# Kernel tuning notes

Measured on AMD Instinct MI355X. Metric: run time of the kernel, lower is better.

Reference implementation:

```python
import jax, jax.numpy as jnp
import numpy as np

HID = 768          # args.hidden_size
LSTM2 = 768        # args.lstm_dim * 2
SCALE = HID ** -0.5


def _cross_attn(q_in, kv_in, Wq, bq, Wk, bk, Wv, bv):
    # Linear projections (weights stored as [in, out])
    Q = q_in @ Wq + bq            # [B, Sq, H]
    K = kv_in @ Wk + bk           # [B, Sk, H]
    V = kv_in @ Wv + bv           # [B, Sk, H]
    attn = jnp.einsum('bqh,bkh->bqk', Q, K) * SCALE
    attn = jax.nn.softmax(attn, axis=-1)
    return jnp.einsum('bqk,bkh->bqh', attn, V)


def setup_inputs() -> dict:
    key = jax.random.key(0)
    ks = jax.random.split(key, 14)
    B, Ssyn, Ssem = 4, 4096, 2048
    syntactic_feat = jax.random.normal(ks[0], (B, Ssyn, LSTM2), jnp.float32)
    semantic_feat = jax.random.normal(ks[1], (B, Ssem, HID), jnp.float32)

    def lin(k, fan_in, fan_out):
        kw, kb = jax.random.split(k)
        bound = 1.0 / np.sqrt(fan_in)
        W = jax.random.uniform(kw, (fan_in, fan_out), jnp.float32, -bound, bound)
        b = jax.random.uniform(kb, (fan_out,), jnp.float32, -bound, bound)
        return W, b

    # syntax_to_semantic: query_dim=HID, key_dim=LSTM2
    Wq1, bq1 = lin(ks[2], HID, HID)
    Wk1, bk1 = lin(ks[3], LSTM2, HID)
    Wv1, bv1 = lin(ks[4], LSTM2, HID)
    # semantic_to_syntax: query_dim=LSTM2, key_dim=HID
    Wq2, bq2 = lin(ks[5], LSTM2, HID)
    Wk2, bk2 = lin(ks[6], HID, HID)
    Wv2, bv2 = lin(ks[7], HID, HID)
    return dict(syntactic_feat=syntactic_feat, semantic_feat=semantic_feat,
                Wq1=Wq1, bq1=bq1, Wk1=Wk1, bk1=bk1, Wv1=Wv1, bv1=bv1,
                Wq2=Wq2, bq2=bq2, Wk2=Wk2, bk2=bk2, Wv2=Wv2, bv2=bv2)


def reference(syntactic_feat, semantic_feat,
              Wq1, bq1, Wk1, bk1, Wv1, bv1,
              Wq2, bq2, Wk2, bk2, Wv2, bv2):
    # enhanced_semantic: queries from semantic, keys/values from syntactic
    enhanced_semantic = _cross_attn(semantic_feat, syntactic_feat,
                                    Wq1, bq1, Wk1, bk1, Wv1, bv1)
    # enhanced_syntax: queries from syntactic, keys/values from semantic
    enhanced_syntax = _cross_attn(syntactic_feat, semantic_feat,
                                  Wq2, bq2, Wk2, bk2, Wv2, bv2)
    return enhanced_semantic, enhanced_syntax
```

## Files before the change

### kernel.cpp

```cpp
#include <hip/hip_runtime.h>
#include <stdint.h>


typedef unsigned short u16;
typedef __attribute__((ext_vector_type(8))) __bf16 bf16x8;
typedef __attribute__((ext_vector_type(4))) float f32x4;

__device__ __forceinline__ float bf2f(u16 u) {
  union { unsigned int i; float f; } x; x.i = ((unsigned int)u) << 16; return x.f;
}
__device__ __forceinline__ u16 f2bf(float f) {
  union { float f; unsigned int i; } x; x.f = f;
  unsigned int i = x.i;
  i += 0x7fffu + ((i >> 16) & 1u);
  return (u16)(i >> 16);
}

__device__ __forceinline__ void cp16(void* lds, const void* g) {
  __builtin_amdgcn_global_load_lds((__attribute__((address_space(1))) void*)g,
                                   (__attribute__((address_space(3))) void*)lds,
                                   16, 0, 0);
}

struct GemmDesc {
  const u16* A; const u16* Bt; const float* bias; void* C;
  long sA, sB, sC;
  int K, lda, ldb, ldc;
  int gx, gy;
  int start, nblk;
  int mode, outf;
  float scale;
};
struct GemmPack { GemmDesc d[6]; int nd; };

#define PHASE(MH, I0, PAR, RDB, STAGE, WAITC)                                 \
  {                                                                           \
    const bf16x8* As8 =                                                       \
        (const bf16x8*)((const char*)L + (PAR) * 32768 + (MH) * 16384);       \
    bf16x8 a0[2][2];                                                          \
    _Pragma("unroll")                                                         \
    for (int s = 0; s < 2; ++s)                                               \
      _Pragma("unroll")                                                       \
      for (int i = 0; i < 2; ++i) a0[s][i] = As8[iaq[s][(I0) + i]];           \
    if (RDB) {                                                                \
      const bf16x8* Bl8 =                                                     \
          (const bf16x8*)((const char*)L + 65536 + (PAR) * 32768);            \
      const bf16x8* Bh8 =                                                     \
          (const bf16x8*)((const char*)L + 65536 + (PAR) * 32768 + 16384);    \
      _Pragma("unroll")                                                       \
      for (int s = 0; s < 2; ++s)                                             \
        _Pragma("unroll")                                                     \
        for (int j = 0; j < 2; ++j) {                                         \
          bfr[0][s][j] = Bl8[ibq[s][j]];                                      \
          bfr[1][s][j] = Bh8[ibq[s][j]];                                      \
        }                                                                     \
    }                                                                         \
    STAGE;                                                                    \
    if (RDB) { asm volatile("s_waitcnt lgkmcnt(8)" ::: "memory"); }           \
    __builtin_amdgcn_s_barrier();                                             \
    asm volatile("s_waitcnt lgkmcnt(0)" ::: "memory");                        \
    __builtin_amdgcn_s_setprio(1);                                            \
    _Pragma("unroll")                                                         \
    for (int s = 0; s < 2; ++s)                                               \
      _Pragma("unroll")                                                       \
      for (int i = 0; i < 2; ++i)                                             \
        _Pragma("unroll")                                                     \
        for (int nh = 0; nh < 2; ++nh)                                        \
          _Pragma("unroll")                                                   \
          for (int j = 0; j < 2; ++j)                                         \
            acc[MH][nh][(I0) + i][j] =                                        \
                __builtin_amdgcn_mfma_f32_16x16x32_bf16(                      \
                    bfr[nh][s][j], a0[s][i], acc[MH][nh][(I0) + i][j],        \
                    0, 0, 0);                                                 \
    __builtin_amdgcn_s_setprio(0);                                            \
    WAITC;                                                                    \
    __builtin_amdgcn_s_barrier();                                             \
  }

__global__ __launch_bounds__(512, 2)
void gemm256_kernel(GemmPack p)
{
  __shared__ __align__(16) u16 L[65536];

  int seg = 0;
#pragma unroll
  for (int t = 1; t < 6; ++t)
    if (t < p.nd && (int)blockIdx.x >= p.d[t].start) seg = t;
  const GemmDesc& g = p.d[seg];
  const int local0 = (int)blockIdx.x - g.start;
  const int local = (local0 & 7) * (g.nblk >> 3) + (local0 >> 3);
  const int pxy = g.gx * g.gy;
  const int bz = local / pxy;
  const int rem = local - bz * pxy;
  const int by = rem / g.gx;
  const int bx = rem - by * g.gx;

  const int tid  = threadIdx.x;
  const int lane = tid & 63;
  const int wave = tid >> 6;
  const int l15  = lane & 15;
  const int quad = lane >> 4;
  const int wm   = wave >> 2;
  const int wn   = wave & 3;

  const char* Ab = (const char*)(g.A + (long)bz * g.sA + (long)bx * 256 * g.lda);
  const char* Bb = (const char*)(g.Bt + (long)bz * g.sB + (long)by * 256 * g.ldb);
  const long ldaB = (long)g.lda * 2;
  const long ldbB = (long)g.ldb * 2;

  const int gchk = (lane & 7) ^ (lane >> 3);
  const char* pa0 = Ab + (long)(wave * 8 + (lane >> 3)) * ldaB + (gchk << 4);
  const char* pb0 = Bb + (long)(wave * 8 + (lane >> 3)) * ldbB + (gchk << 4);
  char* lA = (char*)L + wave * 1024;
  char* lB = (char*)L + 65536 + wave * 1024;

  auto stA = [&](int tile, int h) {
    char* d = lA + (tile & 1) * 32768 + h * 16384;
    const char* s = pa0 + (long)h * 128 * ldaB + ((long)tile << 7);
    cp16(d, s);
    cp16(d + 8192, s + 64 * ldaB);
  };
  auto stB = [&](int tile, int h) {
    char* d = lB + (tile & 1) * 32768 + h * 16384;
    const char* s = pb0 + (long)h * 128 * ldbB + ((long)tile << 7);
    cp16(d, s);
    cp16(d + 8192, s + 64 * ldbB);
  };

  int iaq[2][4], ibq[2][2];
#pragma unroll
  for (int s = 0; s < 2; ++s) {
#pragma unroll
    for (int i = 0; i < 4; ++i)
      iaq[s][i] = (wm * 64 + i * 16 + l15) * 8 + ((s * 4 + quad) ^ (l15 & 7));
#pragma unroll
    for (int j = 0; j < 2; ++j)
      ibq[s][j] = (wn * 32 + j * 16 + l15) * 8 + ((s * 4 + quad) ^ (l15 & 7));
  }

  f32x4 acc[2][2][4][2];
  {
    f32x4 zz = {0.f, 0.f, 0.f, 0.f};
#pragma unroll
    for (int mh = 0; mh < 2; ++mh)
#pragma unroll
      for (int nh = 0; nh < 2; ++nh)
#pragma unroll
        for (int i = 0; i < 4; ++i)
#pragma unroll
          for (int j = 0; j < 2; ++j) acc[mh][nh][i][j] = zz;
  }
  bf16x8 bfr[2][2][2];

  stB(0, 0); stB(0, 1); stA(0, 0); stA(0, 1);
  stB(1, 0); stB(1, 1); stA(1, 0);
  asm volatile("s_waitcnt vmcnt(6)" ::: "memory");
  __builtin_amdgcn_s_barrier();

  const int nt = g.K >> 6;
  const int NI = nt >> 1;
  for (int it = 0; it < NI; ++it) {
    const int t = it * 2;
    const bool m2 = (t + 2) < nt;
    const bool m3 = (t + 3) < nt;
    PHASE(0, 0, 0, 1, stA(t + 1, 1), )
    PHASE(0, 2, 0, 0, if (m2) stB(t + 2, 0), )
    PHASE(1, 0, 0, 0, if (m2) stB(t + 2, 1), )
    PHASE(1, 2, 0, 0, if (m2) stA(t + 2, 0),
          if (m2) { asm volatile("s_waitcnt vmcnt(6)" ::: "memory"); }
          else    { asm volatile("s_waitcnt vmcnt(0)" ::: "memory"); })
    PHASE(0, 0, 1, 1, if (m2) stA(t + 2, 1), )
    PHASE(0, 2, 1, 0, if (m3) stB(t + 3, 0), )
    PHASE(1, 0, 1, 0, if (m3) stB(t + 3, 1), )
    PHASE(1, 2, 1, 0, if (m3) stA(t + 3, 0),
          if (m3)      { asm volatile("s_waitcnt vmcnt(6)" ::: "memory"); }
          else if (m2) { asm volatile("s_waitcnt vmcnt(0)" ::: "memory"); })
  }

  const long cbase = (long)bz * g.sC;
#pragma unroll
  for (int mh = 0; mh < 2; ++mh) {
#pragma unroll
    for (int i = 0; i < 4; ++i) {
      const int row = bx * 256 + mh * 128 + wm * 64 + i * 16 + l15;
      const float rbias = (g.mode == 2) ? g.bias[row] : 0.f;
#pragma unroll
      for (int nh = 0; nh < 2; ++nh) {
#pragma unroll
        for (int j = 0; j < 2; ++j) {
          const int colbase = by * 256 + nh * 128 + wn * 32 + j * 16 + quad * 4;
          float v[4];
#pragma unroll
          for (int r = 0; r < 4; ++r) v[r] = acc[mh][nh][i][j][r] * g.scale;
          if (g.mode == 1) {
            const float4 cb = *(const float4*)(g.bias + colbase);
            v[0] += cb.x; v[1] += cb.y; v[2] += cb.z; v[3] += cb.w;
          } else if (g.mode == 2) {
#pragma unroll
            for (int r = 0; r < 4; ++r) v[r] += rbias;
          }
          const long idx = cbase + (long)row * g.ldc + colbase;
          if (g.outf) {
            float4 st; st.x = v[0]; st.y = v[1]; st.z = v[2]; st.w = v[3];
            *(float4*)((float*)g.C + idx) = st;
          } else {
            uint2 st;
            st.x = (unsigned int)f2bf(v[0]) | ((unsigned int)f2bf(v[1]) << 16);
            st.y = (unsigned int)f2bf(v[2]) | ((unsigned int)f2bf(v[3]) << 16);
            *(uint2*)((u16*)g.C + idx) = st;
          }
        }
      }
    }
  }
}

__global__ __launch_bounds__(256)
void prep_kernel(const float* __restrict__ sa, u16* __restrict__ da, int n8a,
                 const float* __restrict__ sb, u16* __restrict__ db, int n8b,
                 const float* w0, const float* w1, const float* w2,
                 const float* w3, const float* w4, const float* w5,
                 u16* t0, u16* t1, u16* t2, u16* t3, u16* t4, u16* t5)
{
  __shared__ float t[32][33];
  const int b = blockIdx.x;
  const int tid = threadIdx.x;
  if (b < 9216) {
    int idx = b * 256 + tid;
    const float* src; u16* dst; int i;
    if (idx < n8a) { src = sa; dst = da; i = idx; }
    else           { src = sb; dst = db; i = idx - n8a; if (i >= n8b) return; }
    const float4* s4 = (const float4*)src;
    float4 a = s4[i * 2], c = s4[i * 2 + 1];
    uint4 o;
    o.x = (unsigned int)f2bf(a.x) | ((unsigned int)f2bf(a.y) << 16);
    o.y = (unsigned int)f2bf(a.z) | ((unsigned int)f2bf(a.w) << 16);
    o.z = (unsigned int)f2bf(c.x) | ((unsigned int)f2bf(c.y) << 16);
    o.w = (unsigned int)f2bf(c.z) | ((unsigned int)f2bf(c.w) << 16);
    ((uint4*)dst)[i] = o;
    return;
  }
  const int tb = b - 9216;
  const int z  = tb / 576;
  const int r  = tb - z * 576;
  const int byy = r / 24;
  const int bxx = r - byy * 24;
  const float* src; u16* dst;
  switch (z) {
    case 0: src = w0; dst = t0; break;
    case 1: src = w1; dst = t1; break;
    case 2: src = w2; dst = t2; break;
    case 3: src = w3; dst = t3; break;
    case 4: src = w4; dst = t4; break;
    default: src = w5; dst = t5; break;
  }
  const int tx = tid & 31, ty = tid >> 5;
  const int x = bxx * 32 + tx;
  const int y0 = byy * 32;
#pragma unroll
  for (int j = 0; j < 32; j += 8) t[ty + j][tx] = src[(long)(y0 + ty + j) * 768 + x];
  __syncthreads();
  const int x2 = y0 + tx;
#pragma unroll
  for (int j = 0; j < 32; j += 8)
    dst[(long)(bxx * 32 + ty + j) * 768 + x2] = f2bf(t[tx][ty + j]);
}

template <int NV>
__device__ __forceinline__ void softmax_row(u16* row)
{
  __shared__ float red[8];
  const int tid  = threadIdx.x;
  const int lane = tid & 63;
  const int wave = tid >> 6;
  uint4* p4 = (uint4*)row;

  uint4 ld[NV / 8];
#pragma unroll
  for (int c = 0; c < NV / 8; ++c) ld[c] = p4[tid + c * 256];
  float v[NV];
#pragma unroll
  for (int c = 0; c < NV / 8; ++c) {
    unsigned int w[4] = {ld[c].x, ld[c].y, ld[c].z, ld[c].w};
#pragma unroll
    for (int q = 0; q < 4; ++q) {
      v[c * 8 + q * 2]     = bf2f((u16)(w[q] & 0xffffu));
      v[c * 8 + q * 2 + 1] = bf2f((u16)(w[q] >> 16));
    }
  }

  float m = -1e30f;
#pragma unroll
  for (int i = 0; i < NV; ++i) m = fmaxf(m, v[i]);
#pragma unroll
  for (int off = 32; off > 0; off >>= 1) m = fmaxf(m, __shfl_xor(m, off, 64));
  if (lane == 0) red[wave] = m;
  __syncthreads();
  m = fmaxf(fmaxf(red[0], red[1]), fmaxf(red[2], red[3]));

  float s = 0.f;
#pragma unroll
  for (int i = 0; i < NV; ++i) { v[i] = __expf(v[i] - m); s += v[i]; }
#pragma unroll
  for (int off = 32; off > 0; off >>= 1) s += __shfl_xor(s, off, 64);
  if (lane == 0) red[4 + wave] = s;
  __syncthreads();
  s = (red[4] + red[5]) + (red[6] + red[7]);
  const float inv = 1.0f / s;

#pragma unroll
  for (int c = 0; c < NV / 8; ++c) {
    unsigned int w[4];
#pragma unroll
    for (int q = 0; q < 4; ++q) {
      const u16 lo = f2bf(v[c * 8 + q * 2] * inv);
      const u16 hi = f2bf(v[c * 8 + q * 2 + 1] * inv);
      w[q] = (unsigned int)lo | ((unsigned int)hi << 16);
    }
    uint4 st; st.x = w[0]; st.y = w[1]; st.z = w[2]; st.w = w[3];
    p4[tid + c * 256] = st;
  }
}

__global__ __launch_bounds__(256)
void softmax_both_kernel(u16* S1, u16* S2, const u16* cpy_src, u16* cpy_dst)
{
  if (blockIdx.x < 8192) { softmax_row<16>(S1 + (long)blockIdx.x * 4096); return; }
  if (blockIdx.x < 24576) { softmax_row<8>(S2 + (long)(blockIdx.x - 8192) * 2048); return; }
  const long base = (long)(blockIdx.x - 24576) * 512 + threadIdx.x;
  const uint4* s = (const uint4*)cpy_src;
  uint4* d = (uint4*)cpy_dst;
  d[base] = s[base];
  d[base + 256] = s[base + 256];
}


static GemmDesc mkdesc(const void* A, const void* Bt, const float* bias, void* C,
                       long sA, long sB, long sC, int K, int lda, int ldb, int ldc,
                       int M, int N, int nb, int start, int mode, int outf,
                       float scale)
{
  GemmDesc d;
  d.A = (const u16*)A; d.Bt = (const u16*)Bt; d.bias = bias; d.C = C;
  d.sA = sA; d.sB = sB; d.sC = sC;
  d.K = K; d.lda = lda; d.ldb = ldb; d.ldc = ldc;
  d.gx = M / 256; d.gy = N / 256; d.start = start;
  d.nblk = nb * d.gx * d.gy;
  d.mode = mode; d.outf = outf; d.scale = scale;
  return d;
}

extern "C" void kernel_launch(void* const* d_in, const int* in_sizes, int n_in,
                              void* d_out, int out_size, void* d_ws, size_t ws_size,
                              hipStream_t stream)
{
  (void)in_sizes; (void)n_in; (void)out_size; (void)ws_size;
  const float* syn = (const float*)d_in[0];
  const float* sem = (const float*)d_in[1];
  const float* W[6]    = {(const float*)d_in[2], (const float*)d_in[4],  (const float*)d_in[6],
                          (const float*)d_in[8], (const float*)d_in[10], (const float*)d_in[12]};
  const float* bias[6] = {(const float*)d_in[3], (const float*)d_in[5],  (const float*)d_in[7],
                          (const float*)d_in[9], (const float*)d_in[11], (const float*)d_in[13]};
  float* out = (float*)d_out;

  u16* ws   = (u16*)d_ws;
  u16* S1   = ws;
  u16* synb = ws;
  u16* semb = ws + 12582912;
  u16* WT   = ws + 18874368;
  u16* S2   = ws + 33554432;
  u16* V1T  = ws + 67108864;
  u16* Q1   = ws + 79691776;
  u16* V2Tc = ws + 79691776;
  u16* K1  = (u16*)out;
  u16* o1  = (u16*)(out + 6291456);
  u16* Q2  = o1;
  u16* K2  = o1 + 12582912;
  u16* V2T = o1 + 18874368;

  const float SC = 0.036084391824351615f;

  prep_kernel<<<dim3(12672), dim3(256), 0, stream>>>(
      syn, synb, 1572864, sem, semb, 786432,
      W[0], W[1], W[2], W[3], W[4], W[5],
      WT + 0 * 589824, WT + 1 * 589824, WT + 2 * 589824,
      WT + 3 * 589824, WT + 4 * 589824, WT + 5 * 589824);

  {
    GemmPack p; p.nd = 6;
    p.d[0] = mkdesc(synb, WT + 1 * 589824, bias[1], K1, 0, 0, 0,
                    768, 768, 768, 768, 16384, 768, 1, 0, 1, 0, 1.f);
    p.d[1] = mkdesc(synb, WT + 3 * 589824, bias[3], Q2, 0, 0, 0,
                    768, 768, 768, 768, 16384, 768, 1, 192, 1, 0, 1.f);
    p.d[2] = mkdesc(WT + 2 * 589824, synb, bias[2], V1T, 0, 0, 0,
                    768, 768, 768, 16384, 768, 16384, 1, 384, 2, 0, 1.f);
    p.d[3] = mkdesc(semb, WT + 0 * 589824, bias[0], Q1, 0, 0, 0,
                    768, 768, 768, 768, 8192, 768, 1, 576, 1, 0, 1.f);
    p.d[4] = mkdesc(semb, WT + 4 * 589824, bias[4], K2, 0, 0, 0,
                    768, 768, 768, 768, 8192, 768, 1, 672, 1, 0, 1.f);
    p.d[5] = mkdesc(WT + 5 * 589824, semb, bias[5], V2T, 0, 0, 0,
                    768, 768, 768, 8192, 768, 8192, 1, 768, 2, 0, 1.f);
    gemm256_kernel<<<dim3(864), dim3(512), 0, stream>>>(p);
  }

  {
    GemmPack p; p.nd = 2;
    p.d[0] = mkdesc(Q1, K1, nullptr, S1,
                    1572864L, 3145728L, 8388608L,
                    768, 768, 768, 4096, 2048, 4096, 4, 0, 0, 0, SC);
    p.d[1] = mkdesc(Q2, K2, nullptr, S2,
                    3145728L, 1572864L, 8388608L,
                    768, 768, 768, 2048, 4096, 2048, 4, 512, 0, 0, SC);
    gemm256_kernel<<<dim3(1024), dim3(512), 0, stream>>>(p);
  }

  softmax_both_kernel<<<dim3(26112), dim3(256), 0, stream>>>(S1, S2, V2T, V2Tc);

  {
    GemmPack p; p.nd = 2;
    p.d[0] = mkdesc(S1, V1T, nullptr, out,
                    8388608L, 4096L, 1572864L,
                    4096, 4096, 16384, 768, 2048, 768, 4, 0, 0, 1, 1.f);
    p.d[1] = mkdesc(S2, V2Tc, nullptr, out + 6291456,
                    8388608L, 2048L, 3145728L,
                    2048, 2048, 8192, 768, 4096, 768, 4, 96, 0, 1, 1.f);
    gemm256_kernel<<<dim3(288), dim3(512), 0, stream>>>(p);
  }
}
```

Baseline: 566.8 us.

## Split-K the long attention-value GEMM with atomic accumulation and drop block swizzle

The S1·V1 GEMM (K=4096) is split into four K-chunks of 1024, and each chunk accumulates into the fp32 output with atomic adds. The output region is zeroed with a memset beforehand. This raises the final launch from 288 to 576 blocks and balances work against the K=2048 S2·V2 tiles, which are now scheduled first. The XCD-interleaving block remap is removed from all GEMM launches, which may change L2 locality. The atomic epilogue adds extra memory traffic and makes the summation order nondeterministic.

```diff
diff --git a/kernel.cpp b/kernel.cpp
--- a/kernel.cpp
+++ b/kernel.cpp
@@ -27,7 +27,7 @@
   long sA, sB, sC;
   int K, lda, ldb, ldc;
   int gx, gy;
-  int start, nblk;
+  int start, kof;
   int mode, outf;
   float scale;
 };
@@ -87,8 +87,7 @@
   for (int t = 1; t < 6; ++t)
     if (t < p.nd && (int)blockIdx.x >= p.d[t].start) seg = t;
   const GemmDesc& g = p.d[seg];
-  const int local0 = (int)blockIdx.x - g.start;
-  const int local = (local0 & 7) * (g.nblk >> 3) + (local0 >> 3);
+  const int local = (int)blockIdx.x - g.start;
   const int pxy = g.gx * g.gy;
   const int bz = local / pxy;
   const int rem = local - bz * pxy;
@@ -103,8 +102,8 @@
   const int wm   = wave >> 2;
   const int wn   = wave & 3;
 
-  const char* Ab = (const char*)(g.A + (long)bz * g.sA + (long)bx * 256 * g.lda);
-  const char* Bb = (const char*)(g.Bt + (long)bz * g.sB + (long)by * 256 * g.ldb);
+  const char* Ab = (const char*)(g.A + (long)bz * g.sA + (long)bx * 256 * g.lda + g.kof);
+  const char* Bb = (const char*)(g.Bt + (long)bz * g.sB + (long)by * 256 * g.ldb + g.kof);
   const long ldaB = (long)g.lda * 2;
   const long ldbB = (long)g.ldb * 2;
 
@@ -200,9 +199,15 @@
             for (int r = 0; r < 4; ++r) v[r] += rbias;
           }
           const long idx = cbase + (long)row * g.ldc + colbase;
-          if (g.outf) {
+          if (g.outf == 1) {
             float4 st; st.x = v[0]; st.y = v[1]; st.z = v[2]; st.w = v[3];
             *(float4*)((float*)g.C + idx) = st;
+          } else if (g.outf == 2) {
+            float* cp = (float*)g.C + idx;
+            unsafeAtomicAdd(cp + 0, v[0]);
+            unsafeAtomicAdd(cp + 1, v[1]);
+            unsafeAtomicAdd(cp + 2, v[2]);
+            unsafeAtomicAdd(cp + 3, v[3]);
           } else {
             uint2 st;
             st.x = (unsigned int)f2bf(v[0]) | ((unsigned int)f2bf(v[1]) << 16);
@@ -337,15 +342,14 @@
 
 static GemmDesc mkdesc(const void* A, const void* Bt, const float* bias, void* C,
                        long sA, long sB, long sC, int K, int lda, int ldb, int ldc,
-                       int M, int N, int nb, int start, int mode, int outf,
+                       int M, int N, int start, int kof, int mode, int outf,
                        float scale)
 {
   GemmDesc d;
   d.A = (const u16*)A; d.Bt = (const u16*)Bt; d.bias = bias; d.C = C;
   d.sA = sA; d.sB = sB; d.sC = sC;
   d.K = K; d.lda = lda; d.ldb = ldb; d.ldc = ldc;
-  d.gx = M / 256; d.gy = N / 256; d.start = start;
-  d.nblk = nb * d.gx * d.gy;
+  d.gx = M / 256; d.gy = N / 256; d.start = start; d.kof = kof;
   d.mode = mode; d.outf = outf; d.scale = scale;
   return d;
 }
@@ -389,17 +393,17 @@
   {
     GemmPack p; p.nd = 6;
     p.d[0] = mkdesc(synb, WT + 1 * 589824, bias[1], K1, 0, 0, 0,
-                    768, 768, 768, 768, 16384, 768, 1, 0, 1, 0, 1.f);
+                    768, 768, 768, 768, 16384, 768, 0, 0, 1, 0, 1.f);
     p.d[1] = mkdesc(synb, WT + 3 * 589824, bias[3], Q2, 0, 0, 0,
-                    768, 768, 768, 768, 16384, 768, 1, 192, 1, 0, 1.f);
+                    768, 768, 768, 768, 16384, 768, 192, 0, 1, 0, 1.f);
     p.d[2] = mkdesc(WT + 2 * 589824, synb, bias[2], V1T, 0, 0, 0,
-                    768, 768, 768, 16384, 768, 16384, 1, 384, 2, 0, 1.f);
+                    768, 768, 768, 16384, 768, 16384, 384, 0, 2, 0, 1.f);
     p.d[3] = mkdesc(semb, WT + 0 * 589824, bias[0], Q1, 0, 0, 0,
-                    768, 768, 768, 768, 8192, 768, 1, 576, 1, 0, 1.f);
+                    768, 768, 768, 768, 8192, 768, 576, 0, 1, 0, 1.f);
     p.d[4] = mkdesc(semb, WT + 4 * 589824, bias[4], K2, 0, 0, 0,
-                    768, 768, 768, 768, 8192, 768, 1, 672, 1, 0, 1.f);
+                    768, 768, 768, 768, 8192, 768, 672, 0, 1, 0, 1.f);
     p.d[5] = mkdesc(WT + 5 * 589824, semb, bias[5], V2T, 0, 0, 0,
-                    768, 768, 768, 8192, 768, 8192, 1, 768, 2, 0, 1.f);
+                    768, 768, 768, 8192, 768, 8192, 768, 0, 2, 0, 1.f);
     gemm256_kernel<<<dim3(864), dim3(512), 0, stream>>>(p);
   }
 
@@ -407,23 +411,34 @@
     GemmPack p; p.nd = 2;
     p.d[0] = mkdesc(Q1, K1, nullptr, S1,
                     1572864L, 3145728L, 8388608L,
-                    768, 768, 768, 4096, 2048, 4096, 4, 0, 0, 0, SC);
+                    768, 768, 768, 4096, 2048, 4096, 0, 0, 0, 0, SC);
     p.d[1] = mkdesc(Q2, K2, nullptr, S2,
                     3145728L, 1572864L, 8388608L,
-                    768, 768, 768, 2048, 4096, 2048, 4, 512, 0, 0, SC);
+                    768, 768, 768, 2048, 4096, 2048, 512, 0, 0, 0, SC);
     gemm256_kernel<<<dim3(1024), dim3(512), 0, stream>>>(p);
   }
 
+  hipMemsetAsync(out, 0, 25165824, stream);
+
   softmax_both_kernel<<<dim3(26112), dim3(256), 0, stream>>>(S1, S2, V2T, V2Tc);
 
   {
-    GemmPack p; p.nd = 2;
-    p.d[0] = mkdesc(S1, V1T, nullptr, out,
+    GemmPack p; p.nd = 5;
+    p.d[0] = mkdesc(S2, V2Tc, nullptr, out + 6291456,
+                    8388608L, 2048L, 3145728L,
+                    2048, 2048, 8192, 768, 4096, 768, 0, 0, 0, 1, 1.f);
+    p.d[1] = mkdesc(S1, V1T, nullptr, out,
                     8388608L, 4096L, 1572864L,
-                    4096, 4096, 16384, 768, 2048, 768, 4, 0, 0, 1, 1.f);
-    p.d[1] = mkdesc(S2, V2Tc, nullptr, out + 6291456,
-                    8388608L, 2048L, 3145728L,
-                    2048, 2048, 8192, 768, 4096, 768, 4, 96, 0, 1, 1.f);
-    gemm256_kernel<<<dim3(288), dim3(512), 0, stream>>>(p);
-  }
-}
+                    1024, 4096, 16384, 768, 2048, 768, 192, 0, 0, 2, 1.f);
+    p.d[2] = mkdesc(S1, V1T, nullptr, out,
+                    8388608L, 4096L, 1572864L,
+                    1024, 4096, 16384, 768, 2048, 768, 288, 1024, 0, 2, 1.f);
+    p.d[3] = mkdesc(S1, V1T, nullptr, out,
+                    8388608L, 4096L, 1572864L,
+                    1024, 4096, 16384, 768, 2048, 768, 384, 2048, 0, 2, 1.f);
+    p.d[4] = mkdesc(S1, V1T, nullptr, out,
+                    8388608L, 4096L, 1572864L,
+                    1024, 4096, 16384, 768, 2048, 768, 480, 3072, 0, 2, 1.f);
+    gemm256_kernel<<<dim3(576), dim3(512), 0, stream>>>(p);
+  }
+}
```

New measurement: 813.2 us. 43.5% more time.

## Add 128x128-tile GEMM for PV products and drop block-index swizzle

Applied to the files above, without the earlier changes.

Adds a simpler 128x128-tile GEMM kernel (256 threads, single-buffered LDS) and uses it for the two attention-times-V products. The old 256-tile launch produced only 288 blocks, which under-fills the GPU; the new one launches 1152 blocks. It also removes the interleaved block-index remapping in the 256-tile kernel and uses linear block order instead. The new kernel has no double buffering or prefetch, so load latency is exposed on every k-step, and removing the swizzle may change L2 locality for the projection and score GEMMs.

```diff
diff --git a/kernel.cpp b/kernel.cpp
--- a/kernel.cpp
+++ b/kernel.cpp
@@ -27,7 +27,7 @@
   long sA, sB, sC;
   int K, lda, ldb, ldc;
   int gx, gy;
-  int start, nblk;
+  int start;
   int mode, outf;
   float scale;
 };
@@ -87,8 +87,7 @@
   for (int t = 1; t < 6; ++t)
     if (t < p.nd && (int)blockIdx.x >= p.d[t].start) seg = t;
   const GemmDesc& g = p.d[seg];
-  const int local0 = (int)blockIdx.x - g.start;
-  const int local = (local0 & 7) * (g.nblk >> 3) + (local0 >> 3);
+  const int local = (int)blockIdx.x - g.start;
   const int pxy = g.gx * g.gy;
   const int bz = local / pxy;
   const int rem = local - bz * pxy;
@@ -215,6 +214,135 @@
   }
 }
 
+struct G128Desc {
+  const u16* A; const u16* Bt; const float* bias; void* C;
+  long sA, sB, sC;
+  int K, lda, ldb, ldc;
+  int gx, gy;
+  int start;
+  int mode, outf;
+  float scale;
+};
+struct G128Pack { G128Desc d[6]; int nd; };
+
+__global__ __launch_bounds__(256)
+void gemm128_kernel(G128Pack p)
+{
+  __shared__ __align__(16) u16 Asl[128 * 64];
+  __shared__ __align__(16) u16 Bsl[128 * 64];
+
+  int seg = 0;
+#pragma unroll
+  for (int t = 1; t < 6; ++t)
+    if (t < p.nd && (int)blockIdx.x >= p.d[t].start) seg = t;
+  const G128Desc& g = p.d[seg];
+  const int local = (int)blockIdx.x - g.start;
+  const int pxy = g.gx * g.gy;
+  const int bz = local / pxy;
+  const int rem = local - bz * pxy;
+  const int by = rem / g.gx;
+  const int bx = rem - by * g.gx;
+
+  const int tid  = threadIdx.x;
+  const int lane = tid & 63;
+  const int wave = tid >> 6;
+  const int l15  = lane & 15;
+  const int quad = lane >> 4;
+  const int mw   = (wave >> 1) * 64;
+  const int nw   = (wave & 1) * 64;
+
+  const char* Ab = (const char*)(g.A + (long)bz * g.sA + (long)bx * 128 * g.lda);
+  const char* Bb = (const char*)(g.Bt + (long)bz * g.sB + (long)by * 128 * g.ldb);
+
+  const int srow  = wave * 8 + (lane >> 3);
+  const int gchk  = (lane & 7) ^ (lane >> 3);
+  const long ldaB = (long)g.lda * 2;
+  const long ldbB = (long)g.ldb * 2;
+  const char* pa00 = Ab + (long)srow * ldaB + (gchk << 4);
+  const char* pb00 = Bb + (long)srow * ldbB + (gchk << 4);
+  char* ldsA = (char*)Asl + wave * 1024;
+  char* ldsB = (char*)Bsl + wave * 1024;
+
+  int ia[2][4], ib[2][4];
+#pragma unroll
+  for (int s = 0; s < 2; ++s)
+#pragma unroll
+    for (int i = 0; i < 4; ++i) {
+      const int m = mw + i * 16 + l15;
+      ia[s][i] = m * 8 + ((s * 4 + quad) ^ (l15 & 7));
+      const int n = nw + i * 16 + l15;
+      ib[s][i] = n * 8 + ((s * 4 + quad) ^ (l15 & 7));
+    }
+
+  f32x4 acc[4][4];
+  {
+    f32x4 zz = {0.f, 0.f, 0.f, 0.f};
+#pragma unroll
+    for (int i = 0; i < 4; ++i)
+#pragma unroll
+      for (int j = 0; j < 4; ++j) acc[i][j] = zz;
+  }
+
+  const int nk = g.K >> 6;
+  for (int kk = 0; kk < nk; ++kk) {
+    const long kb = (long)kk << 7;
+#pragma unroll
+    for (int r = 0; r < 4; ++r) {
+      cp16(ldsA + r * 4096, pa00 + kb + (long)r * 32 * ldaB);
+      cp16(ldsB + r * 4096, pb00 + kb + (long)r * 32 * ldbB);
+    }
+    __syncthreads();
+
+    const bf16x8* As8 = (const bf16x8*)Asl;
+    const bf16x8* Bs8 = (const bf16x8*)Bsl;
+#pragma unroll
+    for (int s = 0; s < 2; ++s) {
+      bf16x8 a[4], b[4];
+#pragma unroll
+      for (int i = 0; i < 4; ++i) a[i] = As8[ia[s][i]];
+#pragma unroll
+      for (int j = 0; j < 4; ++j) b[j] = Bs8[ib[s][j]];
+#pragma unroll
+      for (int i = 0; i < 4; ++i)
+#pragma unroll
+        for (int j = 0; j < 4; ++j)
+          acc[i][j] = __builtin_amdgcn_mfma_f32_16x16x32_bf16(b[j], a[i], acc[i][j], 0, 0, 0);
+    }
+    __syncthreads();
+  }
+
+  const long cbase = (long)bz * g.sC;
+#pragma unroll
+  for (int i = 0; i < 4; ++i) {
+    const int row = bx * 128 + mw + i * 16 + l15;
+    const float rbias = (g.mode == 2) ? g.bias[row] : 0.f;
+#pragma unroll
+    for (int j = 0; j < 4; ++j) {
+      const int colbase = by * 128 + nw + j * 16 + quad * 4;
+      float v[4];
+#pragma unroll
+      for (int r = 0; r < 4; ++r) v[r] = acc[i][j][r] * g.scale;
+      if (g.mode == 1) {
+        const float4 cb = *(const float4*)(g.bias + colbase);
+        v[0] += cb.x; v[1] += cb.y; v[2] += cb.z; v[3] += cb.w;
+      } else if (g.mode == 2) {
+#pragma unroll
+        for (int r = 0; r < 4; ++r) v[r] += rbias;
+      }
+      const long idx = cbase + (long)row * g.ldc + colbase;
+      if (g.outf) {
+        float4 st; st.x = v[0]; st.y = v[1]; st.z = v[2]; st.w = v[3];
+        *(float4*)((float*)g.C + idx) = st;
+      } else {
+        uint2 st;
+        st.x = (unsigned int)f2bf(v[0]) | ((unsigned int)f2bf(v[1]) << 16);
+        st.y = (unsigned int)f2bf(v[2]) | ((unsigned int)f2bf(v[3]) << 16);
+        *(uint2*)((u16*)g.C + idx) = st;
+      }
+    }
+  }
+}
+
 __global__ __launch_bounds__(256)
 void prep_kernel(const float* __restrict__ sa, u16* __restrict__ da, int n8a,
                  const float* __restrict__ sb, u16* __restrict__ db, int n8b,
@@ -337,15 +465,26 @@
 
 static GemmDesc mkdesc(const void* A, const void* Bt, const float* bias, void* C,
                        long sA, long sB, long sC, int K, int lda, int ldb, int ldc,
-                       int M, int N, int nb, int start, int mode, int outf,
-                       float scale)
+                       int M, int N, int start, int mode, int outf, float scale)
 {
   GemmDesc d;
   d.A = (const u16*)A; d.Bt = (const u16*)Bt; d.bias = bias; d.C = C;
   d.sA = sA; d.sB = sB; d.sC = sC;
   d.K = K; d.lda = lda; d.ldb = ldb; d.ldc = ldc;
   d.gx = M / 256; d.gy = N / 256; d.start = start;
-  d.nblk = nb * d.gx * d.gy;
+  d.mode = mode; d.outf = outf; d.scale = scale;
+  return d;
+}
+
+static G128Desc mk128(const void* A, const void* Bt, const float* bias, void* C,
+                      long sA, long sB, long sC, int K, int lda, int ldb, int ldc,
+                      int M, int N, int start, int mode, int outf, float scale)
+{
+  G128Desc d;
+  d.A = (const u16*)A; d.Bt = (const u16*)Bt; d.bias = bias; d.C = C;
+  d.sA = sA; d.sB = sB; d.sC = sC;
+  d.K = K; d.lda = lda; d.ldb = ldb; d.ldc = ldc;
+  d.gx = M / 128; d.gy = N / 128; d.start = start;
   d.mode = mode; d.outf = outf; d.scale = scale;
   return d;
 }
@@ -389,17 +528,17 @@
   {
     GemmPack p; p.nd = 6;
     p.d[0] = mkdesc(synb, WT + 1 * 589824, bias[1], K1, 0, 0, 0,
-                    768, 768, 768, 768, 16384, 768, 1, 0, 1, 0, 1.f);
+                    768, 768, 768, 768, 16384, 768, 0, 1, 0, 1.f);
     p.d[1] = mkdesc(synb, WT + 3 * 589824, bias[3], Q2, 0, 0, 0,
-                    768, 768, 768, 768, 16384, 768, 1, 192, 1, 0, 1.f);
+                    768, 768, 768, 768, 16384, 768, 192, 1, 0, 1.f);
     p.d[2] = mkdesc(WT + 2 * 589824, synb, bias[2], V1T, 0, 0, 0,
-                    768, 768, 768, 16384, 768, 16384, 1, 384, 2, 0, 1.f);
+                    768, 768, 768, 16384, 768, 16384, 384, 2, 0, 1.f);
     p.d[3] = mkdesc(semb, WT + 0 * 589824, bias[0], Q1, 0, 0, 0,
-                    768, 768, 768, 768, 8192, 768, 1, 576, 1, 0, 1.f);
+                    768, 768, 768, 768, 8192, 768, 576, 1, 0, 1.f);
     p.d[4] = mkdesc(semb, WT + 4 * 589824, bias[4], K2, 0, 0, 0,
-                    768, 768, 768, 768, 8192, 768, 1, 672, 1, 0, 1.f);
+                    768, 768, 768, 768, 8192, 768, 672, 1, 0, 1.f);
     p.d[5] = mkdesc(WT + 5 * 589824, semb, bias[5], V2T, 0, 0, 0,
-                    768, 768, 768, 8192, 768, 8192, 1, 768, 2, 0, 1.f);
+                    768, 768, 768, 8192, 768, 8192, 768, 2, 0, 1.f);
     gemm256_kernel<<<dim3(864), dim3(512), 0, stream>>>(p);
   }
 
@@ -407,23 +546,23 @@
     GemmPack p; p.nd = 2;
     p.d[0] = mkdesc(Q1, K1, nullptr, S1,
                     1572864L, 3145728L, 8388608L,
-                    768, 768, 768, 4096, 2048, 4096, 4, 0, 0, 0, SC);
+                    768, 768, 768, 4096, 2048, 4096, 0, 0, 0, SC);
     p.d[1] = mkdesc(Q2, K2, nullptr, S2,
                     3145728L, 1572864L, 8388608L,
-                    768, 768, 768, 2048, 4096, 2048, 4, 512, 0, 0, SC);
+                    768, 768, 768, 2048, 4096, 2048, 512, 0, 0, SC);
     gemm256_kernel<<<dim3(1024), dim3(512), 0, stream>>>(p);
   }
 
   softmax_both_kernel<<<dim3(26112), dim3(256), 0, stream>>>(S1, S2, V2T, V2Tc);
 
   {
-    GemmPack p; p.nd = 2;
-    p.d[0] = mkdesc(S1, V1T, nullptr, out,
-                    8388608L, 4096L, 1572864L,
-                    4096, 4096, 16384, 768, 2048, 768, 4, 0, 0, 1, 1.f);
-    p.d[1] = mkdesc(S2, V2Tc, nullptr, out + 6291456,
-                    8388608L, 2048L, 3145728L,
-                    2048, 2048, 8192, 768, 4096, 768, 4, 96, 0, 1, 1.f);
-    gemm256_kernel<<<dim3(288), dim3(512), 0, stream>>>(p);
-  }
-}
+    G128Pack p; p.nd = 2;
+    p.d[0] = mk128(S1, V1T, nullptr, out,
+                   8388608L, 4096L, 1572864L,
+                   4096, 4096, 16384, 768, 2048, 768, 0, 0, 1, 1.f);
+    p.d[1] = mk128(S2, V2Tc, nullptr, out + 6291456,
+                   8388608L, 2048L, 3145728L,
+                   2048, 2048, 8192, 768, 4096, 768, 384, 0, 1, 1.f);
+    gemm128_kernel<<<dim3(1152), dim3(256), 0, stream>>>(p);
+  }
+}
```

Result: no change. 570.5 us (+0.7%).
